# Kernel tuning notes

Measured on AMD Instinct MI355X. Metric: run time of the kernel, lower is better.

## Reference

```python
import jax, jax.numpy as jnp
import numpy as np

HID, NBINS = 256, 4
NMIR, NMRNA, B, NP, PD = 2000, 20000, 16, 2048, 1024
EREG, EPM, EPI = 300000, 320000, 32000


def _lin(x, w, b):
    return x @ w.T + b


def _gelu(x):
    # torch nn.GELU default = exact erf formulation
    return jax.nn.gelu(x, approximate=False)


def _ln(x, g, b):
    m = jnp.mean(x, axis=-1, keepdims=True)
    v = jnp.mean((x - m) ** 2, axis=-1, keepdims=True)
    return (x - m) * jax.lax.rsqrt(v + 1e-5) * g + b


def setup_inputs() -> dict:
    key = jax.random.key(0)
    ks = jax.random.split(key, 48)

    def lin_w(i, dout, din):
        s = 1.0 / np.sqrt(din)
        return jax.random.uniform(ks[i], (dout, din), minval=-s, maxval=s, dtype=jnp.float32)

    inp = {}
    inp['emb_mirna'] = jax.random.normal(ks[0], (NMIR, HID), jnp.float32) * 0.02
    inp['emb_mrna'] = jax.random.normal(ks[1], (NMRNA, HID), jnp.float32) * 0.02
    inp['w_mir2mrna'] = jax.random.uniform(ks[2], (EREG,), jnp.float32)
    inp['w_mrna2mir'] = jax.random.uniform(ks[3], (EREG,), jnp.float32)
    inp['w_mrna2pat'] = jax.random.uniform(ks[4], (EPM,), jnp.float32)
    inp['w_mir2pat'] = jax.random.uniform(ks[5], (EPI,), jnp.float32)
    inp['reg_w_mrna'] = lin_w(6, HID, HID)
    inp['reg_b_mrna'] = jnp.zeros((HID,), jnp.float32)
    inp['reg_w_mirna'] = lin_w(7, HID, HID)
    inp['reg_b_mirna'] = jnp.zeros((HID,), jnp.float32)
    inp['proj_w'] = lin_w(8, HID, HID)
    inp['proj_b'] = jnp.zeros((HID,), jnp.float32)
    inp['ln_g'] = jnp.ones((HID,), jnp.float32)
    inp['ln_b'] = jnp.zeros((HID,), jnp.float32)
    inp['omics_w'] = lin_w(9, NBINS, HID)
    inp['omics_b'] = jnp.zeros((NBINS,), jnp.float32)
    inp['wsi_w'] = lin_w(10, HID, PD)
    inp['wsi_b'] = jnp.zeros((HID,), jnp.float32)
    inp['mlp_w'] = lin_w(11, HID, HID)
    inp['mlp_b'] = jnp.zeros((HID,), jnp.float32)
    inp['wln_g'] = jnp.ones((HID,), jnp.float32)
    inp['wln_b'] = jnp.zeros((HID,), jnp.float32)
    inp['fuse_w1'] = lin_w(12, HID, 2 * HID)
    inp['fuse_b1'] = jnp.zeros((HID,), jnp.float32)
    inp['fuse_w2'] = lin_w(13, NBINS, HID)
    inp['fuse_b2'] = jnp.zeros((NBINS,), jnp.float32)
    inp['patches'] = jax.random.normal(ks[14], (B, NP, PD), jnp.float32)
    inp['mask'] = jnp.ones((B, NP), jnp.float32)
    inp['src_mir2mrna'] = jax.random.randint(ks[15], (EREG,), 0, NMIR, jnp.int32)
    inp['dst_mir2mrna'] = jax.random.randint(ks[16], (EREG,), 0, NMRNA, jnp.int32)
    inp['src_mrna2mir'] = jax.random.randint(ks[17], (EREG,), 0, NMRNA, jnp.int32)
    inp['dst_mrna2mir'] = jax.random.randint(ks[18], (EREG,), 0, NMIR, jnp.int32)
    inp['src_mrna2pat'] = jax.random.randint(ks[19], (EPM,), 0, NMRNA, jnp.int32)
    inp['dst_mrna2pat'] = jax.random.randint(ks[20], (EPM,), 0, B, jnp.int32)
    inp['src_mir2pat'] = jax.random.randint(ks[21], (EPI,), 0, NMIR, jnp.int32)
    inp['dst_mir2pat'] = jax.random.randint(ks[22], (EPI,), 0, B, jnp.int32)
    return inp


def reference(emb_mirna, emb_mrna, w_mir2mrna, w_mrna2mir, w_mrna2pat, w_mir2pat,
              reg_w_mrna, reg_b_mrna, reg_w_mirna, reg_b_mirna,
              proj_w, proj_b, ln_g, ln_b, omics_w, omics_b,
              wsi_w, wsi_b, mlp_w, mlp_b, wln_g, wln_b,
              fuse_w1, fuse_b1, fuse_w2, fuse_b2, patches, mask,
              src_mir2mrna, dst_mir2mrna, src_mrna2mir, dst_mrna2mir,
              src_mrna2pat, dst_mrna2pat, src_mir2pat, dst_mir2pat):
    # ---- omics: node embeddings (nid = arange -> full tables) ----
    h_mir, h_mrna = emb_mirna, emb_mrna
    # ---- SimpleRegEncoder: weighted gather-scatter-sum per etype (on ORIGINAL h) ----
    agg_mrna = jax.ops.segment_sum(h_mir[src_mir2mrna] * w_mir2mrna[:, None], dst_mir2mrna, num_segments=NMRNA)
    agg_mir = jax.ops.segment_sum(h_mrna[src_mrna2mir] * w_mrna2mir[:, None], dst_mrna2mir, num_segments=NMIR)
    h_mrna = h_mrna + _gelu(_lin(agg_mrna, reg_w_mrna, reg_b_mrna))  # dropout = identity (eval)
    h_mir = h_mir + _gelu(_lin(agg_mir, reg_w_mirna, reg_b_mirna))
    # ---- PatientReadout: cross_reducer='sum' over both gene->patient etypes ----
    acc = (jax.ops.segment_sum(h_mrna[src_mrna2pat] * w_mrna2pat[:, None], dst_mrna2pat, num_segments=B)
           + jax.ops.segment_sum(h_mir[src_mir2pat] * w_mir2pat[:, None], dst_mir2pat, num_segments=B))
    pat = _ln(_gelu(_lin(acc, proj_w, proj_b)), ln_g, ln_b)  # [B, HID]
    omics_logits = _lin(pat, omics_w, omics_b)  # [B, NBINS]
    # ---- SimpleWSIEncoder ----
    x = _lin(patches, wsi_w, wsi_b)  # [B, NP, HID]
    denom = jnp.clip(jnp.sum(mask, axis=1, keepdims=True), 1.0, None)
    pooled = jnp.sum(x * mask[:, :, None], axis=1) / denom
    pooled = _gelu(_lin(_gelu(pooled), mlp_w, mlp_b))
    wsi = _ln(pooled, wln_g, wln_b)  # [B, HID]
    # ---- fusion head ----
    cat = jnp.concatenate([pat, wsi], axis=-1)  # [B, 2*HID]
    fused = _lin(_gelu(_lin(cat, fuse_w1, fuse_b1)), fuse_w2, fuse_b2)  # [B, NBINS]
    return fused, omics_logits
```

## Files before the change

### kernel.cpp

```cpp
#include <hip/hip_runtime.h>
#include <math.h>

#define HID 256
#define NBINS 4
#define NMIR 2000
#define NMRNA 20000
#define NG (NMRNA + NMIR)
#define BB 16
#define NP 2048
#define PD 1024
#define EREG 300000
#define EPM 320000
#define EPI 32000

typedef __attribute__((ext_vector_type(8))) short bf16x8;
typedef __attribute__((ext_vector_type(4))) float f32x4;

__device__ __forceinline__ float gelu_exact(float x) {
    return 0.5f * x * (1.0f + erff(x * 0.7071067811865475f));
}

__device__ __forceinline__ unsigned short f2b(float f) {
    union { float f; unsigned int u; } v; v.f = f;
    unsigned int u = v.u + 0x7fffu + ((v.u >> 16) & 1u);
    return (unsigned short)(u >> 16);
}

__device__ __forceinline__ float b2f(unsigned short u) {
    union { unsigned int i; float f; } v; v.i = ((unsigned int)u) << 16;
    return v.f;
}

__device__ __forceinline__ float block_reduce_sum(float v, float* red) {
    int c = threadIdx.x;
    red[c] = v;
    __syncthreads();
    for (int st = 128; st > 0; st >>= 1) {
        if (c < st) red[c] += red[c + st];
        __syncthreads();
    }
    float r = red[0];
    __syncthreads();
    return r;
}

__device__ __forceinline__ float kred(float v, float* red, int b, int kk) {
    red[kk * 16 + b] = v;
    __syncthreads();
    for (int st = 8; st >= 1; st >>= 1) {
        if (kk < st) red[kk * 16 + b] += red[(kk + st) * 16 + b];
        __syncthreads();
    }
    float r = red[b];
    __syncthreads();
    return r;
}

#define NBR 128
#define NBP 32
#define PER_R ((2 * EREG + NBR - 1) / NBR)
#define PER_P ((EPM + EPI + NBP - 1) / NBP)

#define FR_POOL 512
#define FR_EMB ((NG * HID) / 4096)
#define FR_F2B ((2 * HID * HID) / 4096)
#define FR_TOTAL (FR_POOL + FR_EMB + FR_F2B + NBR + NBP)

__global__ __launch_bounds__(1024) void k_front(
        const float* __restrict__ patches, const float* __restrict__ mask,
        float* __restrict__ pooled, float* __restrict__ masksum,
        const float* __restrict__ emb_mirna, const float* __restrict__ emb_mrna,
        unsigned short* __restrict__ embB_mir, unsigned short* __restrict__ embB_mrna,
        const float* __restrict__ regwA, const float* __restrict__ regwB,
        unsigned short* __restrict__ wb,
        const int* __restrict__ dR1, const int* __restrict__ dR2,
        const int* __restrict__ sP1, const int* __restrict__ sP2,
        int* __restrict__ histR, int* __restrict__ histP) {
    __shared__ int lh[NG / 2];
    int bid = blockIdx.x;
    int t = threadIdx.x;
    if (bid < FR_POOL) {
        int slice = bid & 31, b = bid >> 5;
        int sub = t >> 8, col = t & 255;
        int p0 = slice * 64 + sub * 16;
        float4 acc = {0.f, 0.f, 0.f, 0.f};
        float msum = 0.f;
#pragma unroll
        for (int pp = 0; pp < 16; pp++) {
            int p = p0 + pp;
            float m = mask[b * NP + p];
            float4 v = ((const float4*)(patches + ((size_t)b * NP + p) * PD))[col];
            msum += m;
            acc.x += m * v.x; acc.y += m * v.y; acc.z += m * v.z; acc.w += m * v.w;
        }
        float* op = pooled + (size_t)b * PD + col * 4;
        atomicAdd(op + 0, acc.x);
        atomicAdd(op + 1, acc.y);
        atomicAdd(op + 2, acc.z);
        atomicAdd(op + 3, acc.w);
        if (col == 0) atomicAdd(&masksum[b], msum);
        return;
    }
    bid -= FR_POOL;
    if (bid < FR_EMB) {
        const size_t NM = (size_t)NMIR * HID;
        size_t e = (size_t)bid * 4096 + t * 4;
        float4 v;
        unsigned short* o;
        if (e < NM) { v = *(const float4*)(emb_mirna + e); o = embB_mir + e; }
        else        { v = *(const float4*)(emb_mrna + (e - NM)); o = embB_mrna + (e - NM); }
        ushort4 u = { f2b(v.x), f2b(v.y), f2b(v.z), f2b(v.w) };
        *(ushort4*)o = u;
        return;
    }
    bid -= FR_EMB;
    if (bid < FR_F2B) {
        const size_t NW = (size_t)HID * HID;
        size_t e = (size_t)bid * 4096 + t * 4;
        float4 v;
        if (e < NW) v = *(const float4*)(regwA + e);
        else v = *(const float4*)(regwB + (e - NW));
        ushort4 u = { f2b(v.x), f2b(v.y), f2b(v.z), f2b(v.w) };
        *(ushort4*)(wb + e) = u;
        return;
    }
    bid -= FR_F2B;
    for (int i = t; i < NG / 2; i += 1024) lh[i] = 0;
    __syncthreads();
    if (bid < NBR) {
        int beg = bid * PER_R, end = min(beg + PER_R, 2 * EREG);
        for (int i = beg + t; i < end; i += 1024) {
            int d = (i < EREG) ? dR1[i] : NMRNA + dR2[i - EREG];
            atomicAdd(&lh[d >> 1], 1u << ((d & 1) << 4));
        }
        __syncthreads();
        int* out = histR + (size_t)bid * NG;
        for (int i = t; i < NG; i += 1024)
            out[i] = (lh[i >> 1] >> ((i & 1) << 4)) & 0xFFFF;
    } else {
        int pb = bid - NBR;
        int beg = pb * PER_P, end = min(beg + PER_P, EPM + EPI);
        for (int i = beg + t; i < end; i += 1024) {
            int g = (i < EPM) ? sP1[i] : NMRNA + sP2[i - EPM];
            atomicAdd(&lh[g >> 1], 1u << ((g & 1) << 4));
        }
        __syncthreads();
        int* out = histP + (size_t)pb * NG;
        for (int i = t; i < NG; i += 1024)
            out[i] = (lh[i >> 1] >> ((i & 1) << 4)) & 0xFFFF;
    }
}

#define CS_B ((NG + 255) / 256)
__global__ __launch_bounds__(256) void k_colsum(
        const int* __restrict__ histR, const int* __restrict__ histP,
        int* __restrict__ baseR, int* __restrict__ baseP,
        int* __restrict__ cntR, int* __restrict__ cntP) {
    int bid = blockIdx.x;
    if (bid < CS_B) {
        int i = bid * 256 + threadIdx.x;
        if (i >= NG) return;
        int run = 0;
        for (int b = 0; b < NBR; b++) {
            baseR[(size_t)b * NG + i] = run;
            run += histR[(size_t)b * NG + i];
        }
        cntR[i] = run;
    } else {
        int i = (bid - CS_B) * 256 + threadIdx.x;
        if (i >= NG) return;
        int run = 0;
        for (int b = 0; b < NBP; b++) {
            baseP[(size_t)b * NG + i] = run;
            run += histP[(size_t)b * NG + i];
        }
        cntP[i] = run;
    }
}

__global__ __launch_bounds__(1024) void k_scan_small(
        const int* __restrict__ cntR, const int* __restrict__ cntP,
        int* __restrict__ rowptrR, int* __restrict__ rowptrP) {
    __shared__ int part[1024];
    const int* cnt = blockIdx.x ? cntP : cntR;
    int* rowptr = blockIdx.x ? rowptrP : rowptrR;
    int t = threadIdx.x;
    const int chunk = (NG + 1023) >> 10;
    int beg = t * chunk, end = min(beg + chunk, NG);
    int s = 0;
    for (int i = beg; i < end; i++) s += cnt[i];
    part[t] = s;
    __syncthreads();
    for (int st = 1; st < 1024; st <<= 1) {
        int v = (t >= st) ? part[t - st] : 0;
        __syncthreads();
        part[t] += v;
        __syncthreads();
    }
    int off = part[t] - s;
    for (int i = beg; i < end; i++) {
        rowptr[i] = off;
        off += cnt[i];
    }
    if (end == NG) rowptr[NG] = off;
}

__global__ __launch_bounds__(1024) void k_place(
        const int* __restrict__ sR1, const int* __restrict__ dR1, const float* __restrict__ wR1,
        const int* __restrict__ sR2, const int* __restrict__ dR2, const float* __restrict__ wR2,
        const int* __restrict__ sP1, const int* __restrict__ dP1, const float* __restrict__ wP1,
        const int* __restrict__ sP2, const int* __restrict__ dP2, const float* __restrict__ wP2,
        const int* __restrict__ baseR, const int* __restrict__ baseP,
        const int* __restrict__ rowptrR, const int* __restrict__ rowptrP,
        int2* __restrict__ epR, int2* __restrict__ epP) {
    __shared__ int lcur[NG];
    int t = threadIdx.x, bid = blockIdx.x;
    if (bid < NBR) {
        const int* base = baseR + (size_t)bid * NG;
        for (int i = t; i < NG; i += 1024) lcur[i] = rowptrR[i] + base[i];
        __syncthreads();
        int beg = bid * PER_R, end = min(beg + PER_R, 2 * EREG);
        for (int i = beg + t; i < end; i += 1024) {
            int d, s; float w;
            if (i < EREG) { d = dR1[i]; s = sR1[i]; w = wR1[i]; }
            else { int k = i - EREG; d = NMRNA + dR2[k]; s = sR2[k]; w = wR2[k]; }
            int p = atomicAdd(&lcur[d], 1);
            int2 e; e.x = s; e.y = __float_as_int(w);
            epR[p] = e;
        }
    } else {
        int pb = bid - NBR;
        const int* base = baseP + (size_t)pb * NG;
        for (int i = t; i < NG; i += 1024) lcur[i] = rowptrP[i] + base[i];
        __syncthreads();
        int beg = pb * PER_P, end = min(beg + PER_P, EPM + EPI);
        for (int i = beg + t; i < end; i += 1024) {
            int g, b; float w;
            if (i < EPM) { g = sP1[i]; b = dP1[i]; w = wP1[i]; }
            else { int k = i - EPM; g = NMRNA + sP2[k]; b = dP2[k]; w = wP2[k]; }
            int p = atomicAdd(&lcur[g], 1);
            int2 e; e.x = (g << 4) | b; e.y = __float_as_int(w);
            epP[p] = e;
        }
    }
}

__global__ __launch_bounds__(256) void k_gather2(
        const unsigned short* __restrict__ embB_mir, const unsigned short* __restrict__ embB_mrna,
        const int* __restrict__ rowptrR, const int2* __restrict__ epR,
        unsigned short* __restrict__ agg) {
    __shared__ float lacc[4][HID];
    int n = blockIdx.x;
    const unsigned short* emb = (n < NMRNA) ? embB_mir : embB_mrna;
    int wv = threadIdx.x >> 6, l = threadIdx.x & 63;
    int beg = rowptrR[n], end = rowptrR[n + 1];
    float a0 = 0.f, a1 = 0.f, a2 = 0.f, a3 = 0.f;
    float c0 = 0.f, c1 = 0.f, c2 = 0.f, c3 = 0.f;
    float d0 = 0.f, d1 = 0.f, d2 = 0.f, d3 = 0.f;
    float g0 = 0.f, g1 = 0.f, g2 = 0.f, g3 = 0.f;
    int j = beg + wv;
    for (; j + 12 < end; j += 16) {
        int2 e0 = epR[j];
        int2 e1 = epR[j + 4];
        int2 e2 = epR[j + 8];
        int2 e3 = epR[j + 12];
        float w0 = __int_as_float(e0.y), w1 = __int_as_float(e1.y);
        float w2 = __int_as_float(e2.y), w3 = __int_as_float(e3.y);
        ushort4 v0 = *(const ushort4*)(emb + (size_t)e0.x * HID + l * 4);
        ushort4 v1 = *(const ushort4*)(emb + (size_t)e1.x * HID + l * 4);
        ushort4 v2 = *(const ushort4*)(emb + (size_t)e2.x * HID + l * 4);
        ushort4 v3 = *(const ushort4*)(emb + (size_t)e3.x * HID + l * 4);
        a0 += w0 * b2f(v0.x); a1 += w0 * b2f(v0.y); a2 += w0 * b2f(v0.z); a3 += w0 * b2f(v0.w);
        c0 += w1 * b2f(v1.x); c1 += w1 * b2f(v1.y); c2 += w1 * b2f(v1.z); c3 += w1 * b2f(v1.w);
        d0 += w2 * b2f(v2.x); d1 += w2 * b2f(v2.y); d2 += w2 * b2f(v2.z); d3 += w2 * b2f(v2.w);
        g0 += w3 * b2f(v3.x); g1 += w3 * b2f(v3.y); g2 += w3 * b2f(v3.z); g3 += w3 * b2f(v3.w);
    }
    for (; j < end; j += 4) {
        int2 e0 = epR[j];
        float w0 = __int_as_float(e0.y);
        ushort4 v0 = *(const ushort4*)(emb + (size_t)e0.x * HID + l * 4);
        a0 += w0 * b2f(v0.x); a1 += w0 * b2f(v0.y); a2 += w0 * b2f(v0.z); a3 += w0 * b2f(v0.w);
    }
    float4 st = { a0 + c0 + d0 + g0, a1 + c1 + d1 + g1,
                  a2 + c2 + d2 + g2, a3 + c3 + d3 + g3 };
    ((float4*)lacc[wv])[l] = st;
    __syncthreads();
    int c = threadIdx.x;
    agg[(size_t)n * HID + c] = f2b(lacc[0][c] + lacc[1][c] + lacc[2][c] + lacc[3][c]);
}

__global__ __launch_bounds__(256) void k_update2(
        const unsigned short* __restrict__ A,
        const float* __restrict__ emb_mrna, const float* __restrict__ emb_mirna,
        const unsigned short* __restrict__ wb,
        const float* __restrict__ bias_mrna, const float* __restrict__ bias_mirna,
        const int* __restrict__ rowptrP, const int2* __restrict__ epP,
        float* __restrict__ acc_pat) {
    __shared__ float ht[16][HID + 1];
    __shared__ float wtile[16][BB];
    int row0 = blockIdx.x * 16;
    const float* emb; const unsigned short* Wb; const float* bias; int base;
    if (row0 < NMRNA) { emb = emb_mrna;  Wb = wb;             bias = bias_mrna;  base = 0; }
    else              { emb = emb_mirna; Wb = wb + HID * HID; bias = bias_mirna; base = NMRNA; }
    int tid = threadIdx.x;
    if (tid < 16 * BB) wtile[tid >> 4][tid & 15] = 0.f;
    __syncthreads();
    int pbeg = rowptrP[row0], pend = rowptrP[row0 + 16];
    for (int j = pbeg + tid; j < pend; j += 256) {
        int2 e = epP[j];
        atomicAdd(&wtile[(e.x >> 4) - row0][e.x & 15], __int_as_float(e.y));
    }
    int wv = tid >> 6;
    int lane = tid & 63;
    int m = lane & 15;
    int q = lane >> 4;
    bf16x8 afrag[8];
    const unsigned short* arow = A + (size_t)(row0 + m) * HID + q * 8;
#pragma unroll
    for (int kk = 0; kk < 8; kk++)
        afrag[kk] = *(const bf16x8*)(arow + kk * 32);
    f32x4 acc[4];
#pragma unroll
    for (int t = 0; t < 4; t++) acc[t] = (f32x4){0.f, 0.f, 0.f, 0.f};
    int col_base = wv * 64;
#pragma unroll
    for (int t = 0; t < 4; t++) {
        const unsigned short* brow = Wb + (size_t)(col_base + t * 16 + m) * HID + q * 8;
#pragma unroll
        for (int kk = 0; kk < 8; kk++) {
            bf16x8 bfrag = *(const bf16x8*)(brow + kk * 32);
            acc[t] = __builtin_amdgcn_mfma_f32_16x16x32_bf16(afrag[kk], bfrag, acc[t], 0, 0, 0);
        }
    }
#pragma unroll
    for (int t = 0; t < 4; t++) {
        int col = col_base + t * 16 + m;
        float bv = bias[col];
#pragma unroll
        for (int r = 0; r < 4; r++) {
            int lrow = q * 4 + r;
            size_t idxe = (size_t)(row0 - base + lrow) * HID + col;
            ht[lrow][col] = emb[idxe] + gelu_exact(acc[t][r] + bv);
        }
    }
    __syncthreads();
    int c = tid;
    float hv[16];
#pragma unroll
    for (int r = 0; r < 16; r++) hv[r] = ht[r][c];
#pragma unroll
    for (int b = 0; b < BB; b++) {
        float s = 0.f;
#pragma unroll
        for (int r = 0; r < 16; r++) s += wtile[r][b] * hv[r];
        atomicAdd(&acc_pat[b * HID + c], s);
    }
}

__global__ __launch_bounds__(256) void k_head_a(
        const float* __restrict__ acc_pat, const float* __restrict__ pooled,
        const float* __restrict__ masksum,
        const float* __restrict__ proj_w, const float* __restrict__ proj_b,
        const float* __restrict__ wsi_w, const float* __restrict__ wsi_b,
        float* __restrict__ pg, float* __restrict__ wt) {
    __shared__ float red[256];
    int c = blockIdx.x;
    int t = threadIdx.x;
    int b = t & 15, kk = t >> 4;

    const float* wr = proj_w + (size_t)c * HID + kk * 16;
    const float* xr = acc_pat + (size_t)b * HID + kk * 16;
    float s = 0.f;
#pragma unroll
    for (int i = 0; i < 16; i += 4) {
        float4 w4 = *(const float4*)(wr + i);
        float4 x4 = *(const float4*)(xr + i);
        s += x4.x * w4.x + x4.y * w4.y + x4.z * w4.z + x4.w * w4.w;
    }
    float tot = kred(s, red, b, kk);
    if (kk == 0) pg[(size_t)b * HID + c] = gelu_exact(tot + proj_b[c]);

    const float* wr2 = wsi_w + (size_t)c * PD + kk * 64;
    const float* xr2 = pooled + (size_t)b * PD + kk * 64;
    float s2 = 0.f;
#pragma unroll
    for (int i = 0; i < 64; i += 4) {
        float4 w4 = *(const float4*)(wr2 + i);
        float4 x4 = *(const float4*)(xr2 + i);
        s2 += x4.x * w4.x + x4.y * w4.y + x4.z * w4.z + x4.w * w4.w;
    }
    float tot2 = kred(s2, red, b, kk);
    if (kk == 0) {
        float sm = masksum[b];
        float denom = fmaxf(sm, 1.0f);
        wt[(size_t)b * HID + c] = gelu_exact(tot2 / denom + wsi_b[c] * (sm / denom));
    }
}

__global__ __launch_bounds__(256) void k_head_b(
        const float* __restrict__ wt,
        const float* __restrict__ mlp_w, const float* __restrict__ mlp_b,
        float* __restrict__ ml) {
    __shared__ float red[256];
    int c = blockIdx.x;
    int t = threadIdx.x;
    int b = t & 15, kk = t >> 4;
    const float* wr = mlp_w + (size_t)c * HID + kk * 16;
    const float* xr = wt + (size_t)b * HID + kk * 16;
    float s = 0.f;
#pragma unroll
    for (int i = 0; i < 16; i += 4) {
        float4 w4 = *(const float4*)(wr + i);
        float4 x4 = *(const float4*)(xr + i);
        s += x4.x * w4.x + x4.y * w4.y + x4.z * w4.z + x4.w * w4.w;
    }
    float tot = kred(s, red, b, kk);
    if (kk == 0) ml[(size_t)b * HID + c] = gelu_exact(tot + mlp_b[c]);
}

__global__ __launch_bounds__(256) void k_head_c(
        const float* __restrict__ pg, const float* __restrict__ ml,
        const float* __restrict__ ln_g, const float* __restrict__ ln_b,
        const float* __restrict__ wln_g, const float* __restrict__ wln_b,
        const float* __restrict__ omics_w, const float* __restrict__ omics_b,
        const float* __restrict__ fuse_b2,
        float* __restrict__ vecbuf, float* __restrict__ out_omics,
        float* __restrict__ out_fused) {
    __shared__ float red[256];
    int b = blockIdx.x, c = threadIdx.x;
    if (c < NBINS) out_fused[b * NBINS + c] = fuse_b2[c];
    float g = pg[(size_t)b * HID + c];
    float mean = block_reduce_sum(g, red) * (1.0f / HID);
    float d = g - mean;
    float var = block_reduce_sum(d * d, red) * (1.0f / HID);
    float patv = d * rsqrtf(var + 1e-5f) * ln_g[c] + ln_b[c];
    vecbuf[(size_t)b * (2 * HID) + c] = patv;
    for (int o = 0; o < NBINS; o++) {
        float r = block_reduce_sum(patv * omics_w[o * HID + c], red);
        if (c == 0) out_omics[b * NBINS + o] = r + omics_b[o];
    }
    float m = ml[(size_t)b * HID + c];
    mean = block_reduce_sum(m, red) * (1.0f / HID);
    d = m - mean;
    var = block_reduce_sum(d * d, red) * (1.0f / HID);
    vecbuf[(size_t)b * (2 * HID) + HID + c] = d * rsqrtf(var + 1e-5f) * wln_g[c] + wln_b[c];
}

__global__ __launch_bounds__(256) void k_head_d(
        const float* __restrict__ vecbuf,
        const float* __restrict__ fuse_w1, const float* __restrict__ fuse_b1,
        const float* __restrict__ fuse_w2,
        float* __restrict__ out_fused) {
    __shared__ float red[256];
    int c = blockIdx.x;
    int t = threadIdx.x;
    int b = t & 15, kk = t >> 4;
    const float* wr = fuse_w1 + (size_t)c * (2 * HID) + kk * 32;
    const float* xr = vecbuf + (size_t)b * (2 * HID) + kk * 32;
    float s = 0.f;
#pragma unroll
    for (int i = 0; i < 32; i += 4) {
        float4 w4 = *(const float4*)(wr + i);
        float4 x4 = *(const float4*)(xr + i);
        s += x4.x * w4.x + x4.y * w4.y + x4.z * w4.z + x4.w * w4.w;
    }
    float tot = kred(s, red, b, kk);
    if (kk == 0) {
        float h1 = gelu_exact(tot + fuse_b1[c]);
#pragma unroll
        for (int o = 0; o < NBINS; o++)
            atomicAdd(&out_fused[b * NBINS + o], h1 * fuse_w2[o * HID + c]);
    }
}

extern "C" void kernel_launch(void* const* d_in, const int* in_sizes, int n_in,
                              void* d_out, int out_size, void* d_ws, size_t ws_size,
                              hipStream_t stream) {
    const float* emb_mirna  = (const float*)d_in[0];
    const float* emb_mrna   = (const float*)d_in[1];
    const float* w_mir2mrna = (const float*)d_in[2];
    const float* w_mrna2mir = (const float*)d_in[3];
    const float* w_mrna2pat = (const float*)d_in[4];
    const float* w_mir2pat  = (const float*)d_in[5];
    const float* reg_w_mrna = (const float*)d_in[6];
    const float* reg_b_mrna = (const float*)d_in[7];
    const float* reg_w_mirna= (const float*)d_in[8];
    const float* reg_b_mirna= (const float*)d_in[9];
    const float* proj_w     = (const float*)d_in[10];
    const float* proj_b     = (const float*)d_in[11];
    const float* ln_g       = (const float*)d_in[12];
    const float* ln_b       = (const float*)d_in[13];
    const float* omics_w    = (const float*)d_in[14];
    const float* omics_b    = (const float*)d_in[15];
    const float* wsi_w      = (const float*)d_in[16];
    const float* wsi_b      = (const float*)d_in[17];
    const float* mlp_w      = (const float*)d_in[18];
    const float* mlp_b      = (const float*)d_in[19];
    const float* wln_g      = (const float*)d_in[20];
    const float* wln_b      = (const float*)d_in[21];
    const float* fuse_w1    = (const float*)d_in[22];
    const float* fuse_b1    = (const float*)d_in[23];
    const float* fuse_w2    = (const float*)d_in[24];
    const float* fuse_b2    = (const float*)d_in[25];
    const float* patches    = (const float*)d_in[26];
    const float* mask       = (const float*)d_in[27];
    const int* src_m2M = (const int*)d_in[28];
    const int* dst_m2M = (const int*)d_in[29];
    const int* src_M2m = (const int*)d_in[30];
    const int* dst_M2m = (const int*)d_in[31];
    const int* src_M2p = (const int*)d_in[32];
    const int* dst_M2p = (const int*)d_in[33];
    const int* src_m2p = (const int*)d_in[34];
    const int* dst_m2p = (const int*)d_in[35];

    float* ws = (float*)d_ws;
    size_t off = 0;
    float* acc_pat  = ws + off; off += (size_t)BB * HID;
    float* pooled   = ws + off; off += (size_t)BB * PD;
    float* masksum  = ws + off; off += BB;
    size_t zero_floats = off;
    unsigned short* agg_bf = (unsigned short*)(ws + off); off += (size_t)NG * HID / 2;
    unsigned short* wb     = (unsigned short*)(ws + off); off += (size_t)2 * HID * HID / 2;
    unsigned short* embB_mir  = (unsigned short*)(ws + off); off += (size_t)NMIR * HID / 2;
    unsigned short* embB_mrna = (unsigned short*)(ws + off); off += (size_t)NMRNA * HID / 2;
    float* pg       = ws + off; off += (size_t)BB * HID;
    float* wt       = ws + off; off += (size_t)BB * HID;
    float* ml       = ws + off; off += (size_t)BB * HID;
    float* vecbuf   = ws + off; off += (size_t)BB * 2 * HID;
    int* histR      = (int*)(ws + off); off += (size_t)NBR * NG;
    int* histP      = (int*)(ws + off); off += (size_t)NBP * NG;
    int* baseR      = (int*)(ws + off); off += (size_t)NBR * NG;
    int* baseP      = (int*)(ws + off); off += (size_t)NBP * NG;
    int* cntR       = (int*)(ws + off); off += NG;
    int* cntP       = (int*)(ws + off); off += NG;
    int* rowptrR    = (int*)(ws + off); off += NG + 2;
    int* rowptrP    = (int*)(ws + off); off += NG + 2;
    int2* epR       = (int2*)(ws + off); off += (size_t)2 * (2 * EREG);
    int2* epP       = (int2*)(ws + off); off += (size_t)2 * (EPM + EPI);

    float* out_fused = (float*)d_out;
    float* out_omics = (float*)d_out + BB * NBINS;

    hipMemsetAsync(d_ws, 0, zero_floats * sizeof(float), stream);

    k_front<<<FR_TOTAL, 1024, 0, stream>>>(
        patches, mask, pooled, masksum,
        emb_mirna, emb_mrna, embB_mir, embB_mrna,
        reg_w_mrna, reg_w_mirna, wb,
        dst_m2M, dst_M2m, src_M2p, src_m2p, histR, histP);

    k_colsum<<<2 * CS_B, 256, 0, stream>>>(histR, histP, baseR, baseP, cntR, cntP);
    k_scan_small<<<2, 1024, 0, stream>>>(cntR, cntP, rowptrR, rowptrP);
    k_place<<<NBR + NBP, 1024, 0, stream>>>(
        src_m2M, dst_m2M, w_mir2mrna, src_M2m, dst_M2m, w_mrna2mir,
        src_M2p, dst_M2p, w_mrna2pat, src_m2p, dst_m2p, w_mir2pat,
        baseR, baseP, rowptrR, rowptrP, epR, epP);

    k_gather2<<<NG, 256, 0, stream>>>(embB_mir, embB_mrna, rowptrR, epR, agg_bf);

    k_update2<<<NG / 16, 256, 0, stream>>>(agg_bf, emb_mrna, emb_mirna, wb,
                                           reg_b_mrna, reg_b_mirna,
                                           rowptrP, epP, acc_pat);

    k_head_a<<<HID, 256, 0, stream>>>(acc_pat, pooled, masksum,
                                      proj_w, proj_b, wsi_w, wsi_b, pg, wt);
    k_head_b<<<HID, 256, 0, stream>>>(wt, mlp_w, mlp_b, ml);
    k_head_c<<<BB, 256, 0, stream>>>(pg, ml, ln_g, ln_b, wln_g, wln_b,
                                     omics_w, omics_b, fuse_b2,
                                     vecbuf, out_omics, out_fused);
    k_head_d<<<HID, 256, 0, stream>>>(vecbuf, fuse_w1, fuse_b1, fuse_w2, out_fused);
}
```

Before: 519.0 us.

## Replace global atomics with partial buffers and slotted accumulators, drop memset

The patch-pooling blocks now reduce their four sub-rows in shared memory and write per-slice partial sums to a buffer, instead of issuing float atomics to the pooled output. The extra colsum blocks then sum those partials. The patient accumulator is spread over 8 slots to cut atomic contention, and k_head_a sums the slots. Extra k_front blocks zero the slots, which removes the separate memset launch. The cost is more workspace traffic and a slot-summing pass repeated in every k_head_a block.

```diff
diff --git a/kernel.cpp b/kernel.cpp
--- a/kernel.cpp
+++ b/kernel.cpp
@@ -12,6 +12,7 @@
 #define EREG 300000
 #define EPM 320000
 #define EPI 32000
+#define NSLOT 8
 
 typedef __attribute__((ext_vector_type(8))) short bf16x8;
 typedef __attribute__((ext_vector_type(4))) float f32x4;
@@ -64,15 +65,17 @@
 #define FR_POOL 512
 #define FR_EMB ((NG * HID) / 4096)
 #define FR_F2B ((2 * HID * HID) / 4096)
-#define FR_TOTAL (FR_POOL + FR_EMB + FR_F2B + NBR + NBP)
+#define FR_ZACC ((NSLOT * BB * HID) / 4096)
+#define FR_TOTAL (FR_POOL + FR_EMB + FR_F2B + FR_ZACC + NBR + NBP)
 
 __global__ __launch_bounds__(1024) void k_front(
         const float* __restrict__ patches, const float* __restrict__ mask,
-        float* __restrict__ pooled, float* __restrict__ masksum,
+        float* __restrict__ pooled_part, float* __restrict__ maskp,
         const float* __restrict__ emb_mirna, const float* __restrict__ emb_mrna,
         unsigned short* __restrict__ embB_mir, unsigned short* __restrict__ embB_mrna,
         const float* __restrict__ regwA, const float* __restrict__ regwB,
         unsigned short* __restrict__ wb,
+        float* __restrict__ acc_slot,
         const int* __restrict__ dR1, const int* __restrict__ dR2,
         const int* __restrict__ sP1, const int* __restrict__ sP2,
         int* __restrict__ histR, int* __restrict__ histP) {
@@ -80,6 +83,7 @@
     int bid = blockIdx.x;
     int t = threadIdx.x;
     if (bid < FR_POOL) {
+        float* pl = (float*)lh;
         int slice = bid & 31, b = bid >> 5;
         int sub = t >> 8, col = t & 255;
         int p0 = slice * 64 + sub * 16;
@@ -93,12 +97,20 @@
             msum += m;
             acc.x += m * v.x; acc.y += m * v.y; acc.z += m * v.z; acc.w += m * v.w;
         }
-        float* op = pooled + (size_t)b * PD + col * 4;
-        atomicAdd(op + 0, acc.x);
-        atomicAdd(op + 1, acc.y);
-        atomicAdd(op + 2, acc.z);
-        atomicAdd(op + 3, acc.w);
-        if (col == 0) atomicAdd(&masksum[b], msum);
+        ((float4*)pl)[sub * 256 + col] = acc;
+        if (col == 0) pl[4096 + sub] = msum;
+        __syncthreads();
+        if (t < 256) {
+            float4 a0 = ((float4*)pl)[t];
+            float4 a1 = ((float4*)pl)[256 + t];
+            float4 a2 = ((float4*)pl)[512 + t];
+            float4 a3 = ((float4*)pl)[768 + t];
+            float4 s4 = { a0.x + a1.x + a2.x + a3.x, a0.y + a1.y + a2.y + a3.y,
+                          a0.z + a1.z + a2.z + a3.z, a0.w + a1.w + a2.w + a3.w };
+            ((float4*)(pooled_part + ((size_t)slice * 16 + b) * PD))[t] = s4;
+            if (t == 0)
+                maskp[slice * 16 + b] = pl[4096] + pl[4097] + pl[4098] + pl[4099];
+        }
         return;
     }
     bid -= FR_POOL;
@@ -125,6 +137,13 @@
         return;
     }
     bid -= FR_F2B;
+    if (bid < FR_ZACC) {
+        size_t e = (size_t)bid * 4096 + t * 4;
+        float4 z = {0.f, 0.f, 0.f, 0.f};
+        *(float4*)(acc_slot + e) = z;
+        return;
+    }
+    bid -= FR_ZACC;
     for (int i = t; i < NG / 2; i += 1024) lh[i] = 0;
     __syncthreads();
     if (bid < NBR) {
@@ -152,10 +171,13 @@
 }
 
 #define CS_B ((NG + 255) / 256)
+#define PR_B ((BB * PD) / 256)
 __global__ __launch_bounds__(256) void k_colsum(
         const int* __restrict__ histR, const int* __restrict__ histP,
         int* __restrict__ baseR, int* __restrict__ baseP,
-        int* __restrict__ cntR, int* __restrict__ cntP) {
+        int* __restrict__ cntR, int* __restrict__ cntP,
+        const float* __restrict__ pooled_part, const float* __restrict__ maskp,
+        float* __restrict__ pooled, float* __restrict__ masksum) {
     int bid = blockIdx.x;
     if (bid < CS_B) {
         int i = bid * 256 + threadIdx.x;
@@ -166,7 +188,9 @@
             run += histR[(size_t)b * NG + i];
         }
         cntR[i] = run;
-    } else {
+        return;
+    }
+    if (bid < 2 * CS_B) {
         int i = (bid - CS_B) * 256 + threadIdx.x;
         if (i >= NG) return;
         int run = 0;
@@ -175,6 +199,17 @@
             run += histP[(size_t)b * NG + i];
         }
         cntP[i] = run;
+        return;
+    }
+    int pr = bid - 2 * CS_B;
+    int o = pr * 256 + threadIdx.x;
+    float s = 0.f;
+    for (int sl = 0; sl < 32; sl++) s += pooled_part[(size_t)sl * BB * PD + o];
+    pooled[o] = s;
+    if (pr == 0 && threadIdx.x < BB) {
+        float ms = 0.f;
+        for (int sl = 0; sl < 32; sl++) ms += maskp[sl * BB + threadIdx.x];
+        masksum[threadIdx.x] = ms;
     }
 }
 
@@ -295,7 +330,7 @@
         const unsigned short* __restrict__ wb,
         const float* __restrict__ bias_mrna, const float* __restrict__ bias_mirna,
         const int* __restrict__ rowptrP, const int2* __restrict__ epP,
-        float* __restrict__ acc_pat) {
+        float* __restrict__ acc_slot) {
     __shared__ float ht[16][HID + 1];
     __shared__ float wtile[16][BB];
     int row0 = blockIdx.x * 16;
@@ -344,6 +379,7 @@
         }
     }
     __syncthreads();
+    float* out = acc_slot + (size_t)(blockIdx.x & (NSLOT - 1)) * BB * HID;
     int c = tid;
     float hv[16];
 #pragma unroll
@@ -353,29 +389,37 @@
         float s = 0.f;
 #pragma unroll
         for (int r = 0; r < 16; r++) s += wtile[r][b] * hv[r];
-        atomicAdd(&acc_pat[b * HID + c], s);
+        atomicAdd(&out[b * HID + c], s);
     }
 }
 
 __global__ __launch_bounds__(256) void k_head_a(
-        const float* __restrict__ acc_pat, const float* __restrict__ pooled,
+        const float* __restrict__ acc_slot, const float* __restrict__ pooled,
         const float* __restrict__ masksum,
         const float* __restrict__ proj_w, const float* __restrict__ proj_b,
         const float* __restrict__ wsi_w, const float* __restrict__ wsi_b,
         float* __restrict__ pg, float* __restrict__ wt) {
     __shared__ float red[256];
+    __shared__ float accs[BB * (HID + 1)];
     int c = blockIdx.x;
     int t = threadIdx.x;
     int b = t & 15, kk = t >> 4;
 
+    for (int j = t; j < BB * HID; j += 256) {
+        float v = 0.f;
+#pragma unroll
+        for (int s = 0; s < NSLOT; s++) v += acc_slot[(size_t)s * BB * HID + j];
+        accs[(j >> 8) * (HID + 1) + (j & 255)] = v;
+    }
+    __syncthreads();
+
     const float* wr = proj_w + (size_t)c * HID + kk * 16;
-    const float* xr = acc_pat + (size_t)b * HID + kk * 16;
+    const float* ax = accs + b * (HID + 1) + kk * 16;
     float s = 0.f;
 #pragma unroll
     for (int i = 0; i < 16; i += 4) {
         float4 w4 = *(const float4*)(wr + i);
-        float4 x4 = *(const float4*)(xr + i);
-        s += x4.x * w4.x + x4.y * w4.y + x4.z * w4.z + x4.w * w4.w;
+        s += ax[i] * w4.x + ax[i + 1] * w4.y + ax[i + 2] * w4.z + ax[i + 3] * w4.w;
     }
     float tot = kred(s, red, b, kk);
     if (kk == 0) pg[(size_t)b * HID + c] = gelu_exact(tot + proj_b[c]);
@@ -515,10 +559,11 @@
 
     float* ws = (float*)d_ws;
     size_t off = 0;
-    float* acc_pat  = ws + off; off += (size_t)BB * HID;
-    float* pooled   = ws + off; off += (size_t)BB * PD;
-    float* masksum  = ws + off; off += BB;
-    size_t zero_floats = off;
+    float* acc_slot    = ws + off; off += (size_t)NSLOT * BB * HID;
+    float* pooled      = ws + off; off += (size_t)BB * PD;
+    float* masksum     = ws + off; off += BB;
+    float* pooled_part = ws + off; off += (size_t)32 * BB * PD;
+    float* maskp       = ws + off; off += 32 * BB;
     unsigned short* agg_bf = (unsigned short*)(ws + off); off += (size_t)NG * HID / 2;
     unsigned short* wb     = (unsigned short*)(ws + off); off += (size_t)2 * HID * HID / 2;
     unsigned short* embB_mir  = (unsigned short*)(ws + off); off += (size_t)NMIR * HID / 2;
@@ -541,15 +586,15 @@
     float* out_fused = (float*)d_out;
     float* out_omics = (float*)d_out + BB * NBINS;
 
-    hipMemsetAsync(d_ws, 0, zero_floats * sizeof(float), stream);
-
     k_front<<<FR_TOTAL, 1024, 0, stream>>>(
-        patches, mask, pooled, masksum,
+        patches, mask, pooled_part, maskp,
         emb_mirna, emb_mrna, embB_mir, embB_mrna,
-        reg_w_mrna, reg_w_mirna, wb,
+        reg_w_mrna, reg_w_mirna, wb, acc_slot,
         dst_m2M, dst_M2m, src_M2p, src_m2p, histR, histP);
 
-    k_colsum<<<2 * CS_B, 256, 0, stream>>>(histR, histP, baseR, baseP, cntR, cntP);
+    k_colsum<<<2 * CS_B + PR_B, 256, 0, stream>>>(
+        histR, histP, baseR, baseP, cntR, cntP,
+        pooled_part, maskp, pooled, masksum);
     k_scan_small<<<2, 1024, 0, stream>>>(cntR, cntP, rowptrR, rowptrP);
     k_place<<<NBR + NBP, 1024, 0, stream>>>(
         src_m2M, dst_m2M, w_mir2mrna, src_M2m, dst_M2m, w_mrna2mir,
@@ -560,9 +605,9 @@
 
     k_update2<<<NG / 16, 256, 0, stream>>>(agg_bf, emb_mrna, emb_mirna, wb,
                                            reg_b_mrna, reg_b_mirna,
-                                           rowptrP, epP, acc_pat);
-
-    k_head_a<<<HID, 256, 0, stream>>>(acc_pat, pooled, masksum,
+                                           rowptrP, epP, acc_slot);
+
+    k_head_a<<<HID, 256, 0, stream>>>(acc_slot, pooled, masksum,
                                       proj_w, proj_b, wsi_w, wsi_b, pg, wt);
     k_head_b<<<HID, 256, 0, stream>>>(wt, mlp_w, mlp_b, ml);
     k_head_c<<<BB, 256, 0, stream>>>(pg, ml, ln_g, ln_b, wln_g, wln_b,
```

Measured after the change: 500.2 us. 3.6% less time.
